# Kernel tuning notes

Hardware: AMD Instinct MI355X
Metric: run time of the kernel (lower is better)

## Reference

```python
import jax, jax.numpy as jnp
import numpy as np

N, E, D, L = 100000, 640000, 128, 5
BN_EPS = 1e-5


def setup_inputs() -> dict:
    key = jax.random.key(0)
    ks = jax.random.split(key, 10)
    x = jax.random.normal(ks[0], (N, D), jnp.float32)
    edge_index = jax.random.randint(ks[1], (2, E), 0, N, dtype=jnp.int32)
    W1 = jax.random.normal(ks[2], (L, D, 2 * D), jnp.float32) / np.float32(np.sqrt(D))
    b1 = jnp.zeros((L, 2 * D), jnp.float32)
    bn1_g = jnp.ones((L, 2 * D), jnp.float32)
    bn1_b = jnp.zeros((L, 2 * D), jnp.float32)
    bn1_m = 0.1 * jax.random.normal(ks[3], (L, 2 * D), jnp.float32)
    bn1_v = jax.random.uniform(ks[4], (L, 2 * D), jnp.float32) + 0.5
    W2 = jax.random.normal(ks[5], (L, 2 * D, D), jnp.float32) / np.float32(np.sqrt(2 * D))
    b2 = jnp.zeros((L, D), jnp.float32)
    bno_g = jnp.ones((L, D), jnp.float32)
    bno_b = jnp.zeros((L, D), jnp.float32)
    bno_m = 0.1 * jax.random.normal(ks[6], (L, D), jnp.float32)
    bno_v = jax.random.uniform(ks[7], (L, D), jnp.float32) + 0.5
    return {"x": x, "edge_index": edge_index, "W1": W1, "b1": b1,
            "bn1_g": bn1_g, "bn1_b": bn1_b, "bn1_m": bn1_m, "bn1_v": bn1_v,
            "W2": W2, "b2": b2,
            "bno_g": bno_g, "bno_b": bno_b, "bno_m": bno_m, "bno_v": bno_v}


def _bn(z, g, b, m, v):
    # BatchNorm1d in eval mode: running stats
    return (z - m) * jax.lax.rsqrt(v + BN_EPS) * g + b


def reference(x, edge_index, W1, b1, bn1_g, bn1_b, bn1_m, bn1_v,
              W2, b2, bno_g, bno_b, bno_m, bno_v):
    src, dst = edge_index[0], edge_index[1]
    h = x
    for l in range(L):
        # GINConv with eps=0: (1+eps)*h_i + sum_{j->i} h_j
        agg = h + jax.ops.segment_sum(h[src], dst, num_segments=N)  # [N, d]
        z = jax.nn.relu(_bn(agg @ W1[l] + b1[l], bn1_g[l], bn1_b[l], bn1_m[l], bn1_v[l]))
        h = _bn(z @ W2[l] + b2[l], bno_g[l], bno_b[l], bno_m[l], bno_v[l])
        if l != L - 1:
            h = jax.nn.relu(h)
        # dropout is identity in eval mode
    return h
```

## Files before the change

kernel.cpp:

```cpp
#include <hip/hip_runtime.h>

#define ND 100000
#define DD 128
#define HH 256
#define EE 640000
#define LL 5

typedef __attribute__((ext_vector_type(8))) short short8;
typedef __attribute__((ext_vector_type(4))) short short4v;
typedef __attribute__((ext_vector_type(4))) float f32x4;

static __device__ __forceinline__ short f2bf(float f) {
    unsigned u = __builtin_bit_cast(unsigned, f);
    unsigned r = (u + 0x7fffu + ((u >> 16) & 1u)) >> 16;
    return (short)r;
}
static __device__ __forceinline__ float bf2f(short s) {
    unsigned u = ((unsigned)(unsigned short)s) << 16;
    return __builtin_bit_cast(float, u);
}

__global__ __launch_bounds__(256) void setup(
    const float* __restrict__ W1, const float* __restrict__ b1,
    const float* __restrict__ g1, const float* __restrict__ bb1,
    const float* __restrict__ m1, const float* __restrict__ v1,
    const float* __restrict__ W2, const float* __restrict__ b2,
    const float* __restrict__ g2, const float* __restrict__ bb2,
    const float* __restrict__ m2, const float* __restrict__ v2,
    const float* __restrict__ x, const int* __restrict__ dst,
    short* __restrict__ W1p, float* __restrict__ b1e,
    short* __restrict__ W2p, float* __restrict__ b2e,
    short* __restrict__ hb, int* __restrict__ cnt)
{
    int bx = blockIdx.x;
    int tid = threadIdx.x;
    if (bx < 640) {
        int id = bx * 256 + tid;
        if (id < LL * HH * DD) {
            int l = id >> 15;
            int rem = id & 32767;
            {
                int n = rem >> 7, k = rem & 127;
                float s = g1[l * HH + n] * rsqrtf(v1[l * HH + n] + 1e-5f);
                W1p[id] = f2bf(W1[l * 32768 + k * HH + n] * s);
            }
            {
                int n2 = rem >> 8, k2 = rem & 255;
                float s = g2[l * DD + n2] * rsqrtf(v2[l * DD + n2] + 1e-5f);
                W2p[id] = f2bf(W2[l * 32768 + k2 * DD + n2] * s);
            }
        }
        if (id < LL * HH) {
            float s = g1[id] * rsqrtf(v1[id] + 1e-5f);
            b1e[id] = (b1[id] - m1[id]) * s + bb1[id];
        }
        if (id < LL * DD) {
            float s = g2[id] * rsqrtf(v2[id] + 1e-5f);
            b2e[id] = (b2[id] - m2[id]) * s + bb2[id];
        }
    } else if (bx < 13140) {
        int i = (bx - 640) * 256 + tid;
        float4 v = reinterpret_cast<const float4*>(x)[i];
        short4v s;
        s.x = f2bf(v.x); s.y = f2bf(v.y); s.z = f2bf(v.z); s.w = f2bf(v.w);
        reinterpret_cast<short4v*>(hb)[i] = s;
    } else {
        int e = (bx - 13140) * 256 + tid;
        if (e < EE) atomicAdd(&cnt[dst[e]], 1);
    }
}

__global__ __launch_bounds__(256) void zero_counts(int* __restrict__ p)
{
    int i = blockIdx.x * 256 + threadIdx.x;
    if (i * 4 < 2 * ND) {
        int rem = 2 * ND - i * 4;
        if (rem >= 4) reinterpret_cast<int4*>(p)[i] = make_int4(0, 0, 0, 0);
        else for (int j = 0; j < rem; ++j) p[i * 4 + j] = 0;
    }
}

__global__ __launch_bounds__(256) void scan_block(int* __restrict__ cnt, int* __restrict__ bsum)
{
    __shared__ int buf[256];
    int tid = threadIdx.x;
    int idx = blockIdx.x * 256 + tid;
    int v = (idx < ND) ? cnt[idx] : 0;
    buf[tid] = v;
    __syncthreads();
    int sum = v;
    for (int off = 1; off < 256; off <<= 1) {
        int t = (tid >= off) ? buf[tid - off] : 0;
        __syncthreads();
        sum += t;
        buf[tid] = sum;
        __syncthreads();
    }
    if (idx < ND) cnt[idx] = sum;
    if (tid == 255) bsum[blockIdx.x] = sum;
}

__global__ __launch_bounds__(512) void scan_bsum(const int* __restrict__ bsum,
                                                 int* __restrict__ boffs)
{
    __shared__ int buf[512];
    int tid = threadIdx.x;
    int v = (tid < 391) ? bsum[tid] : 0;
    buf[tid] = v;
    __syncthreads();
    int sum = v;
    for (int off = 1; off < 512; off <<= 1) {
        int t = (tid >= off) ? buf[tid - off] : 0;
        __syncthreads();
        sum += t;
        buf[tid] = sum;
        __syncthreads();
    }
    if (tid < 391) boffs[tid] = sum - v;
}

__global__ __launch_bounds__(256) void apply_offs(const int* __restrict__ cnt,
                                                  const int* __restrict__ boffs,
                                                  int* __restrict__ rowst)
{
    int idx = blockIdx.x * 256 + threadIdx.x;
    if (idx < ND) rowst[idx + 1] = cnt[idx] + boffs[blockIdx.x];
    if (idx == 0) rowst[0] = 0;
}

__global__ __launch_bounds__(256) void fill_csr(const int* __restrict__ src,
                                                const int* __restrict__ dst,
                                                const int* __restrict__ rowstart,
                                                int* __restrict__ cursor,
                                                int* __restrict__ csr)
{
    int e = blockIdx.x * 256 + threadIdx.x;
    if (e < EE) {
        int d = dst[e];
        int p = atomicAdd(&cursor[d], 1);
        csr[rowstart[d] + p] = src[e];
    }
}

__global__ __launch_bounds__(256, 4) void layer_fused(
    const short* __restrict__ hb_in,
    const int* __restrict__ rowst,
    const int* __restrict__ csr,
    const short* __restrict__ W1l,
    const float* __restrict__ b1l,
    const short* __restrict__ W2l,
    const float* __restrict__ b2l,
    short* __restrict__ hb_out, float* __restrict__ f_out, int last)
{
    __shared__ __attribute__((aligned(16))) short sU[64 * 264];

    const int tid = threadIdx.x;
    const int r0 = blockIdx.x * 64;
    const int wave = tid >> 6;
    const int lane = tid & 63;
    const int quad = lane >> 4;
    const int l16 = lane & 15;

    for (int p = 0; p < 4; ++p) {
        int t = p * 256 + tid;
        int row = t >> 4;
        int ch = (t & 15) * 8;
        int grow = r0 + row;
        float acc[8];
        if (grow < ND) {
            short8 h0 = *reinterpret_cast<const short8*>(&hb_in[(size_t)grow * DD + ch]);
            for (int j = 0; j < 8; ++j) acc[j] = bf2f(h0[j]);
            int s = rowst[grow], e = rowst[grow + 1];
            int i = s;
            for (; i + 1 < e; i += 2) {
                int s0 = csr[i], s1 = csr[i + 1];
                short8 a = *reinterpret_cast<const short8*>(&hb_in[(size_t)s0 * DD + ch]);
                short8 b = *reinterpret_cast<const short8*>(&hb_in[(size_t)s1 * DD + ch]);
                for (int j = 0; j < 8; ++j) acc[j] += bf2f(a[j]) + bf2f(b[j]);
            }
            if (i < e) {
                short8 a = *reinterpret_cast<const short8*>(&hb_in[(size_t)csr[i] * DD + ch]);
                for (int j = 0; j < 8; ++j) acc[j] += bf2f(a[j]);
            }
        } else {
            for (int j = 0; j < 8; ++j) acc[j] = 0.f;
        }
        short8 o;
        for (int j = 0; j < 8; ++j) o[j] = f2bf(acc[j]);
        *reinterpret_cast<short8*>(&sU[row * 136 + ch]) = o;
    }
    __syncthreads();

    const f32x4 zero4 = {0.f, 0.f, 0.f, 0.f};
    f32x4 acc1[4][4];
    for (int mt = 0; mt < 4; ++mt)
        for (int nt = 0; nt < 4; ++nt) acc1[mt][nt] = zero4;

    const int wb = wave * 64;
    for (int ks = 0; ks < 4; ++ks) {
        int kofs = ks * 32 + quad * 8;
        short8 aw[4], bn[4];
        for (int mt = 0; mt < 4; ++mt)
            aw[mt] = *reinterpret_cast<const short8*>(&W1l[(wb + mt * 16 + l16) * DD + kofs]);
        for (int nt = 0; nt < 4; ++nt)
            bn[nt] = *reinterpret_cast<const short8*>(&sU[(nt * 16 + l16) * 136 + kofs]);
        for (int mt = 0; mt < 4; ++mt)
            for (int nt = 0; nt < 4; ++nt)
                acc1[mt][nt] = __builtin_amdgcn_mfma_f32_16x16x32_bf16(
                    aw[mt], bn[nt], acc1[mt][nt], 0, 0, 0);
    }
    __syncthreads();

    for (int mt = 0; mt < 4; ++mt) {
        int zc = wb + mt * 16 + quad * 4;
        float4 bias = *reinterpret_cast<const float4*>(&b1l[zc]);
        for (int nt = 0; nt < 4; ++nt) {
            int node = nt * 16 + l16;
            short4v o;
            o.x = f2bf(fmaxf(acc1[mt][nt][0] + bias.x, 0.f));
            o.y = f2bf(fmaxf(acc1[mt][nt][1] + bias.y, 0.f));
            o.z = f2bf(fmaxf(acc1[mt][nt][2] + bias.z, 0.f));
            o.w = f2bf(fmaxf(acc1[mt][nt][3] + bias.w, 0.f));
            *reinterpret_cast<short4v*>(&sU[node * 264 + zc]) = o;
        }
    }
    __syncthreads();

    f32x4 acc2[2][4];
    for (int ct = 0; ct < 2; ++ct)
        for (int nt = 0; nt < 4; ++nt) acc2[ct][nt] = zero4;

    const int c2 = wave * 32;
    for (int ks = 0; ks < 8; ++ks) {
        int kofs = ks * 32 + quad * 8;
        short8 aw[2], bn[4];
        for (int ct = 0; ct < 2; ++ct)
            aw[ct] = *reinterpret_cast<const short8*>(&W2l[(c2 + ct * 16 + l16) * HH + kofs]);
        for (int nt = 0; nt < 4; ++nt)
            bn[nt] = *reinterpret_cast<const short8*>(&sU[(nt * 16 + l16) * 264 + kofs]);
        for (int ct = 0; ct < 2; ++ct)
            for (int nt = 0; nt < 4; ++nt)
                acc2[ct][nt] = __builtin_amdgcn_mfma_f32_16x16x32_bf16(
                    aw[ct], bn[nt], acc2[ct][nt], 0, 0, 0);
    }

    for (int ct = 0; ct < 2; ++ct) {
        int oc = c2 + ct * 16 + quad * 4;
        float4 bias = *reinterpret_cast<const float4*>(&b2l[oc]);
        for (int nt = 0; nt < 4; ++nt) {
            int node = r0 + nt * 16 + l16;
            if (node < ND) {
                float v0 = acc2[ct][nt][0] + bias.x;
                float v1 = acc2[ct][nt][1] + bias.y;
                float v2 = acc2[ct][nt][2] + bias.z;
                float v3 = acc2[ct][nt][3] + bias.w;
                if (!last) {
                    short4v o;
                    o.x = f2bf(fmaxf(v0, 0.f));
                    o.y = f2bf(fmaxf(v1, 0.f));
                    o.z = f2bf(fmaxf(v2, 0.f));
                    o.w = f2bf(fmaxf(v3, 0.f));
                    *reinterpret_cast<short4v*>(&hb_out[(size_t)node * DD + oc]) = o;
                } else {
                    float4 st; st.x = v0; st.y = v1; st.z = v2; st.w = v3;
                    *reinterpret_cast<float4*>(&f_out[(size_t)node * DD + oc]) = st;
                }
            }
        }
    }
}

extern "C" void kernel_launch(void* const* d_in, const int* in_sizes, int n_in,
                              void* d_out, int out_size, void* d_ws, size_t ws_size,
                              hipStream_t stream)
{
    const float* x  = (const float*)d_in[0];
    const int* ei   = (const int*)d_in[1];
    const int* src  = ei;
    const int* dst  = ei + EE;
    const float* W1 = (const float*)d_in[2];
    const float* b1 = (const float*)d_in[3];
    const float* g1 = (const float*)d_in[4];
    const float* bb1= (const float*)d_in[5];
    const float* m1 = (const float*)d_in[6];
    const float* v1 = (const float*)d_in[7];
    const float* W2 = (const float*)d_in[8];
    const float* b2 = (const float*)d_in[9];
    const float* g2 = (const float*)d_in[10];
    const float* bb2= (const float*)d_in[11];
    const float* m2 = (const float*)d_in[12];
    const float* v2 = (const float*)d_in[13];

    char* w = (char*)d_ws;
    short* hbufA = (short*)w;
    short* hbufB = (short*)(w + 25600000);
    short* W1p   = (short*)(w + 51200000);
    short* W2p   = (short*)(w + 51527680);
    float* b1e   = (float*)(w + 51855360);
    float* b2e   = (float*)(w + 51860480);
    int*   cnt   = (int*)  (w + 51863040);
    int*   cursor= (int*)  (w + 52263040);
    int*   rowst = (int*)  (w + 52663040);
    int*   csr   = (int*)  (w + 53063072);
    int*   bsum  = (int*)  (w + 55623072);
    int*   boffs = (int*)  (w + 55624736);
    float* out   = (float*)d_out;

    zero_counts<<<196, 256, 0, stream>>>(cnt);
    setup<<<15640, 256, 0, stream>>>(W1, b1, g1, bb1, m1, v1,
                                     W2, b2, g2, bb2, m2, v2,
                                     x, dst, W1p, b1e, W2p, b2e, hbufA, cnt);
    scan_block<<<391, 256, 0, stream>>>(cnt, bsum);
    scan_bsum<<<1, 512, 0, stream>>>(bsum, boffs);
    apply_offs<<<391, 256, 0, stream>>>(cnt, boffs, rowst);
    fill_csr<<<2500, 256, 0, stream>>>(src, dst, rowst, cursor, csr);

    short* hin = hbufA;
    short* hout = hbufB;
    for (int l = 0; l < LL; ++l) {
        layer_fused<<<1563, 256, 0, stream>>>(hin, rowst, csr,
                                              W1p + l * 32768, b1e + l * HH,
                                              W2p + l * 32768, b2e + l * DD,
                                              hout, out, (l == LL - 1) ? 1 : 0);
        short* t = hin; hin = hout; hout = t;
    }
}
```

Before: 555.7 us.

## Use 1024-thread blocks in fused GIN layer, one node-row per thread

The fused layer kernel now runs 1024 threads per block instead of 256. Each thread gathers neighbours for a single row-chunk instead of looping four times, and each of the 16 waves computes a smaller MFMA tile for both GEMMs. This raises parallelism for the latency-bound neighbour gather and cuts per-thread register use. The cost is more block-wide barriers across 16 waves and weight fragments loaded redundantly across waves. The count zeroing kernel is also replaced by hipMemsetAsync.

After: 569.4 us. 1.02x slower.

```diff
diff --git a/kernel.cpp b/kernel.cpp
--- a/kernel.cpp
+++ b/kernel.cpp
@@ -70,16 +70,6 @@
     }
 }
 
-__global__ __launch_bounds__(256) void zero_counts(int* __restrict__ p)
-{
-    int i = blockIdx.x * 256 + threadIdx.x;
-    if (i * 4 < 2 * ND) {
-        int rem = 2 * ND - i * 4;
-        if (rem >= 4) reinterpret_cast<int4*>(p)[i] = make_int4(0, 0, 0, 0);
-        else for (int j = 0; j < rem; ++j) p[i * 4 + j] = 0;
-    }
-}
-
 __global__ __launch_bounds__(256) void scan_block(int* __restrict__ cnt, int* __restrict__ bsum)
 {
     __shared__ int buf[256];
@@ -142,7 +132,7 @@
     }
 }
 
-__global__ __launch_bounds__(256, 4) void layer_fused(
+__global__ __launch_bounds__(1024, 8) void layer_fused(
     const short* __restrict__ hb_in,
     const int* __restrict__ rowst,
     const int* __restrict__ csr,
@@ -161,10 +151,9 @@
     const int quad = lane >> 4;
     const int l16 = lane & 15;
 
-    for (int p = 0; p < 4; ++p) {
-        int t = p * 256 + tid;
-        int row = t >> 4;
-        int ch = (t & 15) * 8;
+    {
+        int row = tid >> 4;
+        int ch = (tid & 15) * 8;
         int grow = r0 + row;
         float acc[8];
         if (grow < ND) {
@@ -192,68 +181,61 @@
     __syncthreads();
 
     const f32x4 zero4 = {0.f, 0.f, 0.f, 0.f};
-    f32x4 acc1[4][4];
-    for (int mt = 0; mt < 4; ++mt)
-        for (int nt = 0; nt < 4; ++nt) acc1[mt][nt] = zero4;
-
-    const int wb = wave * 64;
+    f32x4 acc1[4];
+    for (int nt = 0; nt < 4; ++nt) acc1[nt] = zero4;
+
+    const int zrow = wave * 16 + l16;
     for (int ks = 0; ks < 4; ++ks) {
         int kofs = ks * 32 + quad * 8;
-        short8 aw[4], bn[4];
-        for (int mt = 0; mt < 4; ++mt)
-            aw[mt] = *reinterpret_cast<const short8*>(&W1l[(wb + mt * 16 + l16) * DD + kofs]);
-        for (int nt = 0; nt < 4; ++nt)
-            bn[nt] = *reinterpret_cast<const short8*>(&sU[(nt * 16 + l16) * 136 + kofs]);
-        for (int mt = 0; mt < 4; ++mt)
-            for (int nt = 0; nt < 4; ++nt)
-                acc1[mt][nt] = __builtin_amdgcn_mfma_f32_16x16x32_bf16(
-                    aw[mt], bn[nt], acc1[mt][nt], 0, 0, 0);
-    }
-    __syncthreads();
-
-    for (int mt = 0; mt < 4; ++mt) {
-        int zc = wb + mt * 16 + quad * 4;
+        short8 aw = *reinterpret_cast<const short8*>(&W1l[zrow * DD + kofs]);
+        for (int nt = 0; nt < 4; ++nt) {
+            short8 bn = *reinterpret_cast<const short8*>(&sU[(nt * 16 + l16) * 136 + kofs]);
+            acc1[nt] = __builtin_amdgcn_mfma_f32_16x16x32_bf16(aw, bn, acc1[nt], 0, 0, 0);
+        }
+    }
+    __syncthreads();
+
+    {
+        int zc = wave * 16 + quad * 4;
         float4 bias = *reinterpret_cast<const float4*>(&b1l[zc]);
         for (int nt = 0; nt < 4; ++nt) {
             int node = nt * 16 + l16;
             short4v o;
-            o.x = f2bf(fmaxf(acc1[mt][nt][0] + bias.x, 0.f));
-            o.y = f2bf(fmaxf(acc1[mt][nt][1] + bias.y, 0.f));
-            o.z = f2bf(fmaxf(acc1[mt][nt][2] + bias.z, 0.f));
-            o.w = f2bf(fmaxf(acc1[mt][nt][3] + bias.w, 0.f));
+            o.x = f2bf(fmaxf(acc1[nt][0] + bias.x, 0.f));
+            o.y = f2bf(fmaxf(acc1[nt][1] + bias.y, 0.f));
+            o.z = f2bf(fmaxf(acc1[nt][2] + bias.z, 0.f));
+            o.w = f2bf(fmaxf(acc1[nt][3] + bias.w, 0.f));
             *reinterpret_cast<short4v*>(&sU[node * 264 + zc]) = o;
         }
     }
     __syncthreads();
 
-    f32x4 acc2[2][4];
-    for (int ct = 0; ct < 2; ++ct)
-        for (int nt = 0; nt < 4; ++nt) acc2[ct][nt] = zero4;
-
-    const int c2 = wave * 32;
+    f32x4 acc2[2];
+    for (int nt = 0; nt < 2; ++nt) acc2[nt] = zero4;
+
+    const int ct16 = wave >> 1;
+    const int nh = wave & 1;
+    const int orow = ct16 * 16 + l16;
     for (int ks = 0; ks < 8; ++ks) {
         int kofs = ks * 32 + quad * 8;
-        short8 aw[2], bn[4];
-        for (int ct = 0; ct < 2; ++ct)
-            aw[ct] = *reinterpret_cast<const short8*>(&W2l[(c2 + ct * 16 + l16) * HH + kofs]);
-        for (int nt = 0; nt < 4; ++nt)
-            bn[nt] = *reinterpret_cast<const short8*>(&sU[(nt * 16 + l16) * 264 + kofs]);
-        for (int ct = 0; ct < 2; ++ct)
-            for (int nt = 0; nt < 4; ++nt)
-                acc2[ct][nt] = __builtin_amdgcn_mfma_f32_16x16x32_bf16(
-                    aw[ct], bn[nt], acc2[ct][nt], 0, 0, 0);
-    }
-
-    for (int ct = 0; ct < 2; ++ct) {
-        int oc = c2 + ct * 16 + quad * 4;
+        short8 aw = *reinterpret_cast<const short8*>(&W2l[orow * HH + kofs]);
+        for (int nt = 0; nt < 2; ++nt) {
+            int node = nh * 32 + nt * 16 + l16;
+            short8 bn = *reinterpret_cast<const short8*>(&sU[node * 264 + kofs]);
+            acc2[nt] = __builtin_amdgcn_mfma_f32_16x16x32_bf16(aw, bn, acc2[nt], 0, 0, 0);
+        }
+    }
+
+    {
+        int oc = ct16 * 16 + quad * 4;
         float4 bias = *reinterpret_cast<const float4*>(&b2l[oc]);
-        for (int nt = 0; nt < 4; ++nt) {
-            int node = r0 + nt * 16 + l16;
+        for (int nt = 0; nt < 2; ++nt) {
+            int node = r0 + nh * 32 + nt * 16 + l16;
             if (node < ND) {
-                float v0 = acc2[ct][nt][0] + bias.x;
-                float v1 = acc2[ct][nt][1] + bias.y;
-                float v2 = acc2[ct][nt][2] + bias.z;
-                float v3 = acc2[ct][nt][3] + bias.w;
+                float v0 = acc2[nt][0] + bias.x;
+                float v1 = acc2[nt][1] + bias.y;
+                float v2 = acc2[nt][2] + bias.z;
+                float v3 = acc2[nt][3] + bias.w;
                 if (!last) {
                     short4v o;
                     o.x = f2bf(fmaxf(v0, 0.f));
@@ -306,7 +288,7 @@
     int*   boffs = (int*)  (w + 55624736);
     float* out   = (float*)d_out;
 
-    zero_counts<<<196, 256, 0, stream>>>(cnt);
+    hipMemsetAsync(cnt, 0, 800000, stream);
     setup<<<15640, 256, 0, stream>>>(W1, b1, g1, bb1, m1, v1,
                                      W2, b2, g2, bb2, m2, v2,
                                      x, dst, W1p, b1e, W2p, b2e, hbufA, cnt);
@@ -318,10 +300,10 @@
     short* hin = hbufA;
     short* hout = hbufB;
     for (int l = 0; l < LL; ++l) {
-        layer_fused<<<1563, 256, 0, stream>>>(hin, rowst, csr,
-                                              W1p + l * 32768, b1e + l * HH,
-                                              W2p + l * 32768, b2e + l * DD,
-                                              hout, out, (l == LL - 1) ? 1 : 0);
+        layer_fused<<<1563, 1024, 0, stream>>>(hin, rowst, csr,
+                                               W1p + l * 32768, b1e + l * HH,
+                                               W2p + l * 32768, b2e + l * DD,
+                                               hout, out, (l == LL - 1) ? 1 : 0);
         short* t = hin; hin = hout; hout = t;
     }
 }
```
